# Kernel optimization log

Hardware: AMD Instinct MI355X
Metric: run time of the kernel (lower is better)

## Reference

```python
import jax, jax.numpy as jnp
import numpy as np

L, B, T, N, C, H, K, M = 2, 4, 8, 2048, 2, 64, 3, 32
DIN0, DIN1, DOUT = C + H, 2 * H, 4 * H


def setup_inputs() -> dict:
    key = jax.random.key(0)
    ks = jax.random.split(key, 24)
    s = 0.05
    p = lambda k, shape: jax.random.normal(k, shape, jnp.float32) * s
    return {
        # support matrices, roughly row-normalized random graph
        "G": jax.random.uniform(ks[0], (K, N, N), jnp.float32) * (2.0 / N),
        "x_seq": jax.random.normal(ks[1], (B, T, N, C), jnp.float32),
        "init_h": jnp.zeros((L, B, N, H), jnp.float32),
        "init_c": jnp.zeros((L, B, N, H), jnp.float32),
        "x_meta": jax.random.normal(ks[2], (B, T, M), jnp.float32),
        # layer 0 meta-learner params (dim_in = C+H)
        "lw1_0": p(ks[3], (M, 64)), "lb1_0": p(ks[4], (64,)),
        "lw2_0": p(ks[5], (64, K * DIN0 * DOUT)), "lb2_0": p(ks[6], (K * DIN0 * DOUT,)),
        "bw1_0": p(ks[7], (M, 64)), "bb1_0": p(ks[8], (64,)),
        "bw2_0": p(ks[9], (64, DOUT)), "bb2_0": p(ks[10], (DOUT,)),
        # layer 1 meta-learner params (dim_in = 2H)
        "lw1_1": p(ks[11], (M, 64)), "lb1_1": p(ks[12], (64,)),
        "lw2_1": p(ks[13], (64, K * DIN1 * DOUT)), "lb2_1": p(ks[14], (K * DIN1 * DOUT,)),
        "bw1_1": p(ks[15], (M, 64)), "bb1_1": p(ks[16], (64,)),
        "bw2_1": p(ks[17], (64, DOUT)), "bb2_1": p(ks[18], (DOUT,)),
    }


def _meta_gcn(G, x, meta, lw1, lb1, lw2, lb2, bw1, bb1, bw2, bb2):
    # x: [B, N, din] -> out: [B, N, 4H]
    Bb, Nn, din = x.shape
    # K-hop supports, concatenated along feature dim (k-major, matches torch.cat)
    sup = jnp.einsum('kij,bjd->bikd', G, x).reshape(Bb, Nn, K * din)
    W = (jax.nn.relu(meta @ lw1 + lb1) @ lw2 + lb2).reshape(Bb, K * din, DOUT)
    b = (jax.nn.relu(meta @ bw1 + bb1) @ bw2 + bb2)[:, None, :]
    return jnp.einsum('bnd,bdo->bno', sup, W) + b


def _run_layer(G, xs_t, meta_t, h0, c0, params):
    # xs_t: [T, B, N, din_x], meta_t: [T, B, M]
    def step(carry, inp):
        h, c = carry
        x_t, m_t = inp
        conv = _meta_gcn(G, jnp.concatenate([x_t, h], axis=-1), m_t, *params)
        gi, gf, go, gg = jnp.split(conv, 4, axis=-1)
        c_t = jax.nn.sigmoid(gf) * c + jax.nn.sigmoid(gi) * jnp.tanh(gg)
        h_t = jax.nn.sigmoid(go) * jnp.tanh(c_t)
        return (h_t, c_t), h_t
    (hT, cT), hs = jax.lax.scan(step, (h0, c0), (xs_t, meta_t))
    return hT, cT, hs


def reference(G, x_seq, init_h, init_c, x_meta,
              lw1_0, lb1_0, lw2_0, lb2_0, bw1_0, bb1_0, bw2_0, bb2_0,
              lw1_1, lb1_1, lw2_1, lb2_1, bw1_1, bb1_1, bw2_1, bb2_1):
    xs = jnp.transpose(x_seq, (1, 0, 2, 3))      # [T, B, N, C]
    ms = jnp.transpose(x_meta, (1, 0, 2))        # [T, B, M]
    p0 = (lw1_0, lb1_0, lw2_0, lb2_0, bw1_0, bb1_0, bw2_0, bb2_0)
    p1 = (lw1_1, lb1_1, lw2_1, lb2_1, bw1_1, bb1_1, bw2_1, bb2_1)
    h0T, c0T, hs0 = _run_layer(G, xs, ms, init_h[0], init_c[0], p0)
    h1T, c1T, _ = _run_layer(G, hs0, ms, init_h[1], init_c[1], p1)
    # [2, L, B, N, H]: [final h per layer; final c per layer]
    return jnp.stack([jnp.stack([h0T, h1T]), jnp.stack([c0T, c1T])])
```

## Files before the change

kernel.cpp:

```cpp
#include <hip/hip_runtime.h>
#include <hip/hip_bf16.h>
#include <cstdint>


typedef __hip_bfloat16 bf16;
typedef __attribute__((ext_vector_type(8))) short bf16x8;
typedef __attribute__((ext_vector_type(4))) short s16x4;
typedef __attribute__((ext_vector_type(4)))  float f32x4;
typedef __attribute__((ext_vector_type(16))) float f32x16;
typedef __attribute__((ext_vector_type(4)))  int   i32x4;
typedef __attribute__((ext_vector_type(16))) int   i32x16;

__device__ __forceinline__ short f2bf(float f) {
    unsigned u = __builtin_bit_cast(unsigned, f);
    return (short)((u + 0x7fffu + ((u >> 16) & 1u)) >> 16);
}

#define GLD_LDS(gaddr, laddr)                                                  \
    __builtin_amdgcn_global_load_lds(                                          \
        (const __attribute__((address_space(1))) void*)(gaddr),                \
        (__attribute__((address_space(3))) void*)(laddr), 16, 0, 0)

#define OFF_GSW    0u
#define OFF_GI8    25165824u
#define OFF_HFA0   37748736u
#define OFF_HFA1   38273024u
#define OFF_HFB0   38797312u
#define OFF_HFB1   39321600u
#define OFF_XS0T   39845888u
#define OFF_HS0F   40370176u
#define OFF_S0X    48758784u
#define OFF_W0SW   74711040u
#define OFF_W1SW   79429632u
#define OFF_BIAS0  85721088u
#define OFF_BIAS1  85753856u
#define OFF_C0     85786624u
#define OFF_C1     87883776u
#define WS_NEEDED  89980928u

__global__ __launch_bounds__(256) void prep_kernel(
    const float* __restrict__ G, const float* __restrict__ x_seq,
    const float* __restrict__ init_h, const float* __restrict__ init_c,
    bf16* __restrict__ Gsw, long* __restrict__ Gi8,
    long* __restrict__ hfA0, long* __restrict__ hfA1,
    bf16* __restrict__ Xs0T, float* __restrict__ c0, float* __restrict__ c1)
{
    const int T_GSB = 1572864;
    const int T_GI8 = 1572864;
    const int T_HF  = 131072;
    const int T_XS  = 262144;
    const int T_C   = 1048576;
    const int TOTAL = T_GSB + T_GI8 + T_HF + T_XS + T_C;
    int stride = gridDim.x * 256;
    for (int idx = blockIdx.x*256 + threadIdx.x; idx < TOTAL; idx += stride) {
        int i0 = idx;
        if (i0 < T_GSB) {
            int lane = i0 & 63, jc = (i0 >> 6) & 127, it32 = (i0 >> 13) & 63, k = i0 >> 19;
            int row = it32*32 + (lane & 31);
            int col = jc*16 + (lane >> 5)*8;
            const float* gp = G + ((size_t)(k*2048 + row))*2048 + col;
            f32x4 v0 = *(const f32x4*)gp, v1 = *(const f32x4*)(gp + 4);
            bf16x8 o;
            #pragma unroll
            for (int e = 0; e < 4; e++) { o[e] = f2bf(v0[e]); o[e+4] = f2bf(v1[e]); }
            *(bf16x8*)((short*)Gsw + (size_t)i0*8) = o;
            continue;
        }
        i0 -= T_GSB;
        if (i0 < T_GI8) {
            int lane = i0 & 63, jc = (i0 >> 6) & 127, it32 = (i0 >> 13) & 63, k = i0 >> 19;
            int row = it32*32 + (lane & 31);
            int col = jc*16 + (lane >> 5)*8;
            const float* gp = G + ((size_t)(k*2048 + row))*2048 + col;
            f32x4 v0 = *(const f32x4*)gp, v1 = *(const f32x4*)(gp + 4);
            long r = 0;
            #pragma unroll
            for (int e = 0; e < 4; e++) {
                int q0 = __float2int_rn(v0[e] * 130048.0f);
                int q1 = __float2int_rn(v1[e] * 130048.0f);
                q0 = q0 < 0 ? 0 : (q0 > 127 ? 127 : q0);
                q1 = q1 < 0 ? 0 : (q1 > 127 ? 127 : q1);
                r |= ((long)(unsigned char)(char)q0) << (8*e);
                r |= ((long)(unsigned char)(char)q1) << (8*(e+4));
            }
            Gi8[i0] = r;
            continue;
        }
        i0 -= T_GI8;
        if (i0 < T_HF) {
            int lane = i0 & 63, dc = (i0 >> 6) & 1, jc = (i0 >> 7) & 127;
            int b = (i0 >> 14) & 3, L = i0 >> 16;
            int j0 = jc*16 + (lane >> 5)*8, d = dc*32 + (lane & 31);
            long r = 0;
            #pragma unroll
            for (int e = 0; e < 8; e++) {
                float hv = init_h[((size_t)(L*4 + b)*2048 + j0 + e)*64 + d];
                int q = __float2int_rn(hv * 127.0f);
                q = q < -127 ? -127 : (q > 127 ? 127 : q);
                r |= ((long)(unsigned char)(char)q) << (8*e);
            }
            long* dst = (L == 0) ? hfA0 : hfA1;
            dst[i0 & 65535] = r;
            continue;
        }
        i0 -= T_HF;
        if (i0 < T_XS) {
            int n = i0 >> 11, j = i0 & 2047;
            float v = 0.f;
            if (n < 64) {
                int t = n >> 3, rm = n & 7, b = rm >> 1, cc = rm & 1;
                v = x_seq[(((size_t)b*8 + t)*2048 + j)*2 + cc];
            }
            Xs0T[i0] = __float2bfloat16(v);
            continue;
        }
        i0 -= T_XS;
        if (i0 < 524288) { c0[i0] = init_c[i0]; continue; }
        i0 -= 524288;
        c1[i0] = init_c[524288 + i0];
    }
}

__global__ __launch_bounds__(256) void metaw_kernel(
    const float* __restrict__ x_meta,
    const float* __restrict__ lw1_0, const float* __restrict__ lb1_0,
    const float* __restrict__ lw2_0, const float* __restrict__ lb2_0,
    const float* __restrict__ bw1_0, const float* __restrict__ bb1_0,
    const float* __restrict__ bw2_0, const float* __restrict__ bb2_0,
    const float* __restrict__ lw1_1, const float* __restrict__ lb1_1,
    const float* __restrict__ lw2_1, const float* __restrict__ lb2_1,
    const float* __restrict__ bw1_1, const float* __restrict__ bb1_1,
    const float* __restrict__ bw2_1, const float* __restrict__ bb2_1,
    bf16* __restrict__ W0sw, bf16* __restrict__ W1sw,
    float* __restrict__ bias0, float* __restrict__ bias1)
{
    int tid = threadIdx.x, bid = blockIdx.x;
    const float *w1, *b1v, *w2, *b2v;
    int task, r = 0;
    if (bid < 384)      { task = 0; r = bid;       w1=lw1_1; b1v=lb1_1; w2=lw2_1; b2v=lb2_1; }
    else if (bid < 582) { task = 1; r = bid - 384; w1=lw1_0; b1v=lb1_0; w2=lw2_0; b2v=lb2_0; }
    else if (bid == 582){ task = 2;                w1=bw1_0; b1v=bb1_0; w2=bw2_0; b2v=bb2_0; }
    else                { task = 3;                w1=bw1_1; b1v=bb1_1; w2=bw2_1; b2v=bb2_1; }

    __shared__ float hid[32][64];
    for (int idx = tid; idx < 2048; idx += 256) {
        int tb = idx >> 6, h = idx & 63;
        int tt = tb >> 2, b = tb & 3;
        float a = b1v[h];
        #pragma unroll
        for (int m = 0; m < 32; m++)
            a += x_meta[((size_t)b*8 + tt)*32 + m] * w1[m*64 + h];
        hid[tb][h] = fmaxf(a, 0.f);
    }
    __syncthreads();

    int o = tid;
    int RO = (task == 0) ? 98304 : (task == 1) ? 50688 : 256;
    int ro = (task >= 2) ? o : (r*256 + o);
    float col[64];
    #pragma unroll
    for (int h = 0; h < 64; h++) col[h] = w2[(size_t)h*RO + ro];
    float base = b2v[ro];

    for (int tb = 0; tb < 32; tb++) {
        float v = base;
        #pragma unroll
        for (int h = 0; h < 64; h++) v += hid[tb][h]*col[h];
        if (task == 0) {
            int rp = r, rc = rp >> 5, rr = rp & 31;
            int oc = o >> 4, l = ((rr >> 3) << 4) + (o & 15), e = rr & 7;
            W1sw[(((size_t)tb*12 + rc)*16 + oc)*512 + l*8 + e] = __float2bfloat16(v);
        } else if (task == 1) {
            int k = r/66, d = r - k*66;
            int rp = k*96 + (d < 2 ? 64 + d : d - 2);
            int rc = rp >> 5, rr = rp & 31;
            int oc = o >> 4, l = ((rr >> 3) << 4) + (o & 15), e = rr & 7;
            W0sw[(((size_t)tb*9 + rc)*16 + oc)*512 + l*8 + e] = __float2bfloat16(v);
        } else if (task == 2) bias0[tb*256 + o] = v;
        else                  bias1[tb*256 + o] = v;
    }
}

__global__ __launch_bounds__(256) void s0x_kernel(
    const short* __restrict__ Gsw, const short* __restrict__ Bm,
    bf16* __restrict__ dstB)
{
    __shared__ short lB[128 * 64];
    int bid = blockIdx.x;
    int mt = (bid & 7) * 6 + (bid >> 3);
    int kk = mt >> 4;

    int tid = threadIdx.x, lane = tid & 63, w = tid >> 6;
    int wr = w >> 1, wc = w & 1;
    int l31 = lane & 31, lhi = lane >> 5;

    int rloc = lane >> 3;
    int gsrc = ((lane & 7) ^ rloc) * 8;
    const short* Bb = Bm + gsrc;

    f32x16 acc[2][2];
    #pragma unroll
    for (int a2 = 0; a2 < 2; a2++)
        #pragma unroll
        for (int b2 = 0; b2 < 2; b2++)
            #pragma unroll
            for (int q = 0; q < 16; q++) acc[a2][b2][q] = 0.f;

    for (int kb = 0; kb < 2048; kb += 64) {
        #pragma unroll
        for (int q = 0; q < 4; q++) {
            int row = (w * 4 + q) * 8 + rloc;
            GLD_LDS(Bb + (size_t)row * 2048 + kb, &lB[(w * 4 + q) * 512]);
        }
        __syncthreads();
        #pragma unroll
        for (int ks = 0; ks < 4; ks++) {
            int jc = (kb >> 4) + ks;
            bf16x8 af[2], bf2[2];
            #pragma unroll
            for (int a2 = 0; a2 < 2; a2++) {
                int it32 = (mt & 15) * 4 + wr * 2 + a2;
                af[a2] = *(const bf16x8*)(Gsw +
                    ((((size_t)(kk * 64 + it32)) * 128 + jc) * 64 + lane) * 8);
            }
            #pragma unroll
            for (int b2 = 0; b2 < 2; b2++) {
                int r = wc * 64 + b2 * 32 + l31;
                int cb = (ks * 32 + lhi * 16) ^ ((r & 7) << 4);
                bf2[b2] = *(const bf16x8*)((const char*)lB + r * 128 + cb);
            }
            #pragma unroll
            for (int a2 = 0; a2 < 2; a2++)
                #pragma unroll
                for (int b2 = 0; b2 < 2; b2++)
                    acc[a2][b2] = __builtin_amdgcn_mfma_f32_32x32x16_bf16(
                        af[a2], bf2[b2], acc[a2][b2], 0, 0, 0);
        }
        __syncthreads();
    }

    #pragma unroll
    for (int a2 = 0; a2 < 2; a2++) {
        #pragma unroll
        for (int b2 = 0; b2 < 2; b2++) {
            int gn = wc * 64 + b2 * 32 + l31;
            if (gn >= 64) continue;
            #pragma unroll
            for (int reg = 0; reg < 16; reg++) {
                int gm = (mt & 15) * 128 + wr * 64 + a2 * 32
                         + (reg & 3) + 8 * (reg >> 2) + 4 * lhi;
                dstB[((size_t)kk * 2048 + gm) * 64 + gn] =
                    __float2bfloat16(acc[a2][b2][reg]);
            }
        }
    }
}

#define LD(P, JC)                                                              \
    do { _Pragma("unroll") for (int k = 0; k < 3; k++)                         \
            P##a[k] = Gi8[(((size_t)(k * 64 + it)) * 128 + (JC)) * 64 + lane]; \
         _Pragma("unroll") for (int dc = 0; dc < 2; dc++)                      \
            P##b[dc] = Bfr[(((size_t)(b * 128 + (JC))) * 2 + dc) * 64 + lane]; \
    } while (0)

#define CP(P)                                                                  \
    do { _Pragma("unroll") for (int k = 0; k < 3; k++)                         \
         _Pragma("unroll") for (int dc = 0; dc < 2; dc++)                      \
            acc6[k * 2 + dc] = __builtin_amdgcn_mfma_i32_32x32x16_i8(          \
                P##a[k], P##b[dc], acc6[k * 2 + dc], 0, 0, 0);                 \
    } while (0)

__device__ __forceinline__ void i8_pass(
    i32x16* acc6, const long* __restrict__ Gi8, const long* __restrict__ Bfr,
    int it, int b, int lane, int w)
{
    #pragma unroll
    for (int f = 0; f < 6; f++)
        #pragma unroll
        for (int r = 0; r < 16; r++) acc6[f][r] = 0;
    int jc0 = w * 32;
    long fAa[3], fAb[2], fBa[3], fBb[2], fCa[3], fCb[2], fDa[3], fDb[2];
    LD(fA, jc0 + 0); LD(fB, jc0 + 1); LD(fC, jc0 + 2); LD(fD, jc0 + 3);
    #pragma unroll 1
    for (int j4 = 0; j4 < 7; j4++) {
        CP(fA); LD(fA, jc0 + j4 * 4 + 4);
        CP(fB); LD(fB, jc0 + j4 * 4 + 5);
        CP(fC); LD(fC, jc0 + j4 * 4 + 6);
        CP(fD); LD(fD, jc0 + j4 * 4 + 7);
    }
    CP(fA); CP(fB); CP(fC); CP(fD);
}

__device__ __forceinline__ void reduce_sup(
    char* lds, char* SUP, i32x16* acc6, int w, int lane)
{
    int* RB = (int*)lds;
    int l31 = lane & 31, lhi = lane >> 5;
    if (w >= 2) {
        #pragma unroll
        for (int f = 0; f < 6; f++)
            #pragma unroll
            for (int qq = 0; qq < 4; qq++) {
                i32x4 v;
                #pragma unroll
                for (int r = 0; r < 4; r++) v[r] = acc6[f][qq * 4 + r];
                *(i32x4*)(RB + ((size_t)((w - 2) * 6 + f)) * 1024 + lane * 16 + qq * 4) = v;
            }
    }
    __syncthreads();
    if (w < 2) {
        #pragma unroll
        for (int f = 0; f < 6; f++)
            #pragma unroll
            for (int r = 0; r < 16; r++)
                acc6[f][r] += RB[((size_t)(w * 6 + f)) * 1024 + lane * 16 + r];
    }
    __syncthreads();
    if (w == 1) {
        #pragma unroll
        for (int f = 0; f < 6; f++)
            #pragma unroll
            for (int qq = 0; qq < 4; qq++) {
                i32x4 v;
                #pragma unroll
                for (int r = 0; r < 4; r++) v[r] = acc6[f][qq * 4 + r];
                *(i32x4*)(RB + (size_t)f * 1024 + lane * 16 + qq * 4) = v;
            }
    }
    __syncthreads();
    if (w == 0) {
        const float SCL = 1.0f / 16516096.0f;
        #pragma unroll
        for (int f = 0; f < 6; f++) {
            int k = f >> 1, dc = f & 1;
            #pragma unroll
            for (int reg = 0; reg < 16; reg++) {
                int s = acc6[f][reg] + RB[(size_t)f * 1024 + lane * 16 + reg];
                float sf = (float)s * SCL;
                int i = (reg & 3) + 8 * (reg >> 2) + 4 * lhi;
                int dpos = k * 64 + dc * 32 + l31;
                *(short*)(SUP + i * 512 + ((dpos * 2) ^ ((i & 15) << 4))) = f2bf(sf);
            }
        }
    }
    __syncthreads();
}

template<int LAYER>
__device__ __forceinline__ void step_part(
    char* lds, int idx, int t,
    const long* __restrict__ Gi8, const short* __restrict__ Sstat,
    const long* __restrict__ hs0f, const short* __restrict__ Wsw,
    const float* __restrict__ bias, float* __restrict__ cbuf,
    const long* __restrict__ hfr_in, long* __restrict__ hfr_out,
    long* __restrict__ hs0f_out, float* __restrict__ out)
{
    constexpr int NC = (LAYER == 0) ? 9 : 12;
    char* SUPs = lds + 24576;
    char* SUPr = lds + 49152;
    short* hT = (short*)(lds + 65536);
    char* hTq = lds + 69632;

    int tid = threadIdx.x, lane = tid & 63, w = tid >> 6;
    int q = idx >> 3;
    int it = (idx & 7) * 8 + (q >> 2), b = q & 3;
    int i0 = it * 32;
    int l15 = lane & 15, lg = lane >> 4;

    i32x16 acc6[6];

    if (LAYER == 0) {
        i8_pass(acc6, Gi8, hfr_in, it, b, lane, w);
        reduce_sup(lds, SUPs, acc6, w, lane);
    } else {
        i8_pass(acc6, Gi8, hfr_in, it, b, lane, w);
        reduce_sup(lds, SUPr, acc6, w, lane);
        i8_pass(acc6, Gi8, hs0f + (size_t)t * 65536, it, b, lane, w);
        reduce_sup(lds, SUPs, acc6, w, lane);
    }

    f32x4 ag[2][4];
    #pragma unroll
    for (int mi = 0; mi < 2; mi++)
        #pragma unroll
        for (int g = 0; g < 4; g++)
            #pragma unroll
            for (int r = 0; r < 4; r++) ag[mi][g][r] = 0.f;

    const short* WswT = Wsw + (size_t)(t * 4 + b) * NC * 16 * 512;

    #pragma unroll
    for (int rc = 0; rc < NC; rc++) {
        bf16x8 a0, a1;
        if (LAYER == 1) {
            int kk = rc >> 2, dq = rc & 3;
            const char* S = (dq < 2) ? SUPs : SUPr;
            int dqe = (dq < 2) ? dq : (dq - 2);
            int dpb = (kk * 64 + dqe * 32 + lg * 8) * 2;
            a0 = *(const bf16x8*)(S + l15 * 512 + (dpb ^ (l15 << 4)));
            a1 = *(const bf16x8*)(S + (l15 + 16) * 512 + (dpb ^ (l15 << 4)));
        } else {
            int kk = rc / 3, dd = rc - kk * 3;
            if (dd < 2) {
                int dpb = (kk * 64 + dd * 32 + lg * 8) * 2;
                a0 = *(const bf16x8*)(SUPs + l15 * 512 + (dpb ^ (l15 << 4)));
                a1 = *(const bf16x8*)(SUPs + (l15 + 16) * 512 + (dpb ^ (l15 << 4)));
            } else {
                #pragma unroll
                for (int e = 0; e < 8; e++) { a0[e] = 0; a1[e] = 0; }
                if (lg == 0) {
                    unsigned v0 = *(const unsigned*)(Sstat + ((size_t)kk * 2048 + i0 + l15) * 64 + t * 8 + b * 2);
                    unsigned v1 = *(const unsigned*)(Sstat + ((size_t)kk * 2048 + i0 + 16 + l15) * 64 + t * 8 + b * 2);
                    a0[0] = (short)(v0 & 0xffff); a0[1] = (short)(v0 >> 16);
                    a1[0] = (short)(v1 & 0xffff); a1[1] = (short)(v1 >> 16);
                }
            }
        }
        #pragma unroll
        for (int g = 0; g < 4; g++) {
            bf16x8 wf = *(const bf16x8*)(WswT + (((size_t)rc * 16 + (g * 4 + w)) * 64 + lane) * 8);
            ag[0][g] = __builtin_amdgcn_mfma_f32_16x16x32_bf16(a0, wf, ag[0][g], 0, 0, 0);
            ag[1][g] = __builtin_amdgcn_mfma_f32_16x16x32_bf16(a1, wf, ag[1][g], 0, 0, 0);
        }
    }

    int hcol = w * 16 + l15;
    float bia[4];
    #pragma unroll
    for (int g = 0; g < 4; g++) bia[g] = bias[(t * 4 + b) * 256 + g * 64 + hcol];

    #pragma unroll
    for (int mi = 0; mi < 2; mi++) {
        #pragma unroll
        for (int r = 0; r < 4; r++) {
            int iloc = mi * 16 + lg * 4 + r;
            int i = i0 + iloc;
            float gi = ag[mi][0][r] + bia[0];
            float gf = ag[mi][1][r] + bia[1];
            float go = ag[mi][2][r] + bia[2];
            float gg = ag[mi][3][r] + bia[3];
            size_t cidx = ((size_t)b * 2048 + i) * 64 + hcol;
            float c_old = cbuf[cidx];
            float si = 1.f / (1.f + __expf(-gi));
            float sf = 1.f / (1.f + __expf(-gf));
            float so = 1.f / (1.f + __expf(-go));
            float cn = sf * c_old + si * tanhf(gg);
            float hn = so * tanhf(cn);
            cbuf[cidx] = cn;
            hT[iloc * 64 + hcol] = f2bf(hn);
            int hq = __float2int_rn(hn * 127.0f);
            hq = hq < -127 ? -127 : (hq > 127 ? 127 : hq);
            hTq[iloc * 64 + hcol] = (char)hq;
            if (t == 7) {
                out[(((size_t)LAYER * 4 + b) * 2048 + i) * 64 + hcol]       = hn;
                out[(((size_t)(2 + LAYER) * 4 + b) * 2048 + i) * 64 + hcol] = cn;
            }
        }
    }
    __syncthreads();

    {
        int jh = tid >> 7, dc = (tid >> 6) & 1, lane6 = tid & 63;
        long r = 0;
        #pragma unroll
        for (int e = 0; e < 8; e++)
            r |= ((long)(unsigned char)hTq[(jh * 16 + (lane6 >> 5) * 8 + e) * 64
                                           + dc * 32 + (lane6 & 31)]) << (8 * e);
        size_t fidx = (((size_t)(b * 128 + it * 2 + jh)) * 2 + dc) * 64 + lane6;
        hfr_out[fidx] = r;
        if (LAYER == 0) hs0f_out[(size_t)t * 65536 + fidx] = r;
    }
}

__global__ __launch_bounds__(256) void combo_kernel(
    const long* __restrict__ Gi8, const short* __restrict__ S0x,
    const long* __restrict__ hs0f_c,
    const short* __restrict__ W0sw, const short* __restrict__ W1sw,
    const float* __restrict__ bias0, const float* __restrict__ bias1,
    float* __restrict__ c0, float* __restrict__ c1,
    long* __restrict__ hfA0, long* __restrict__ hfB0,
    long* __restrict__ hfA1, long* __restrict__ hfB1,
    long* __restrict__ hs0f, float* __restrict__ out, int tau)
{
    __shared__ char lds[71680];
    int bid = blockIdx.x;
    if (bid < 256) {
        int t = tau;
        if (t > 7) return;
        const long* hin  = (t & 1) ? hfB0 : hfA0;
        long*       hout = (t & 1) ? hfA0 : hfB0;
        step_part<0>(lds, bid, t, Gi8, S0x, nullptr, W0sw, bias0, c0,
                     hin, hout, hs0f, out);
    } else {
        int t = tau - 1;
        if (t < 0) return;
        const long* hin  = (t & 1) ? hfB1 : hfA1;
        long*       hout = (t & 1) ? hfA1 : hfB1;
        step_part<1>(lds, bid - 256, t, Gi8, nullptr, hs0f_c, W1sw, bias1, c1,
                     hin, hout, nullptr, out);
    }
}

extern "C" void kernel_launch(void* const* d_in, const int* in_sizes, int n_in,
                              void* d_out, int out_size, void* d_ws, size_t ws_size,
                              hipStream_t stream)
{
    const float* G      = (const float*)d_in[0];
    const float* x_seq  = (const float*)d_in[1];
    const float* init_h = (const float*)d_in[2];
    const float* init_c = (const float*)d_in[3];
    const float* x_meta = (const float*)d_in[4];
    const float* lw1_0 = (const float*)d_in[5],  *lb1_0 = (const float*)d_in[6];
    const float* lw2_0 = (const float*)d_in[7],  *lb2_0 = (const float*)d_in[8];
    const float* bw1_0 = (const float*)d_in[9],  *bb1_0 = (const float*)d_in[10];
    const float* bw2_0 = (const float*)d_in[11], *bb2_0 = (const float*)d_in[12];
    const float* lw1_1 = (const float*)d_in[13], *lb1_1 = (const float*)d_in[14];
    const float* lw2_1 = (const float*)d_in[15], *lb2_1 = (const float*)d_in[16];
    const float* bw1_1 = (const float*)d_in[17], *bb1_1 = (const float*)d_in[18];
    const float* bw2_1 = (const float*)d_in[19], *bb2_1 = (const float*)d_in[20];

    if (ws_size < WS_NEEDED) return;

    char* ws = (char*)d_ws;
    bf16*  Gsw   = (bf16*) (ws + OFF_GSW);
    long*  Gi8   = (long*) (ws + OFF_GI8);
    long*  hfA0  = (long*) (ws + OFF_HFA0);
    long*  hfA1  = (long*) (ws + OFF_HFA1);
    long*  hfB0  = (long*) (ws + OFF_HFB0);
    long*  hfB1  = (long*) (ws + OFF_HFB1);
    bf16*  Xs0T  = (bf16*) (ws + OFF_XS0T);
    long*  hs0f  = (long*) (ws + OFF_HS0F);
    bf16*  S0x   = (bf16*) (ws + OFF_S0X);
    bf16*  W0sw  = (bf16*) (ws + OFF_W0SW);
    bf16*  W1sw  = (bf16*) (ws + OFF_W1SW);
    float* bias0 = (float*)(ws + OFF_BIAS0);
    float* bias1 = (float*)(ws + OFF_BIAS1);
    float* c0    = (float*)(ws + OFF_C0);
    float* c1    = (float*)(ws + OFF_C1);
    float* out   = (float*)d_out;

    prep_kernel<<<4096, 256, 0, stream>>>(G, x_seq, init_h, init_c,
                                          Gsw, Gi8, hfA0, hfA1, Xs0T, c0, c1);
    metaw_kernel<<<584, 256, 0, stream>>>(x_meta,
        lw1_0, lb1_0, lw2_0, lb2_0, bw1_0, bb1_0, bw2_0, bb2_0,
        lw1_1, lb1_1, lw2_1, lb2_1, bw1_1, bb1_1, bw2_1, bb2_1,
        W0sw, W1sw, bias0, bias1);

    s0x_kernel<<<48, 256, 0, stream>>>((const short*)Gsw, (const short*)Xs0T, S0x);

    for (int tau = 0; tau < 9; tau++)
        combo_kernel<<<512, 256, 0, stream>>>(Gi8, (const short*)S0x, hs0f,
            (const short*)W0sw, (const short*)W1sw, bias0, bias1, c0, c1,
            hfA0, hfB0, hfA1, hfB1, hs0f, out, tau);
}
```

Baseline: 475.4 us.

## Fuse timestep launches into persistent kernel with grid barrier and register-resident cell state

Replaces the nine per-timestep combo_kernel launches with one persistent kernel of 512 blocks that loops over timesteps and synchronizes through a global atomic counter barrier. The LSTM cell state now lives in registers across steps instead of being read and written in global memory, and the prep copy of init_c is removed. Hidden states are kept per timestep in larger buffers instead of ping-ponging. The aim is to remove launch gaps and c-state traffic. The grid barrier relies on all 512 blocks being co-resident (launch_bounds 256,2 on 256 CUs), which risks deadlock or spin overhead if occupancy falls short.

```diff
diff --git a/kernel.cpp b/kernel.cpp
--- a/kernel.cpp
+++ b/kernel.cpp
@@ -23,34 +23,31 @@
 
 #define OFF_GSW    0u
 #define OFF_GI8    25165824u
-#define OFF_HFA0   37748736u
-#define OFF_HFA1   38273024u
-#define OFF_HFB0   38797312u
-#define OFF_HFB1   39321600u
-#define OFF_XS0T   39845888u
-#define OFF_HS0F   40370176u
-#define OFF_S0X    48758784u
-#define OFF_W0SW   74711040u
-#define OFF_W1SW   79429632u
-#define OFF_BIAS0  85721088u
-#define OFF_BIAS1  85753856u
-#define OFF_C0     85786624u
-#define OFF_C1     87883776u
-#define WS_NEEDED  89980928u
+#define OFF_HR0    37748736u
+#define OFF_HR1    42467328u
+#define OFF_HS0F   47185920u
+#define OFF_XS0T   51380224u
+#define OFF_S0X    51904512u
+#define OFF_W0SW   52690944u
+#define OFF_W1SW   57409536u
+#define OFF_BIAS0  63700992u
+#define OFF_BIAS1  63733760u
+#define OFF_BAR    63766528u
+#define WS_NEEDED  63767552u
 
 __global__ __launch_bounds__(256) void prep_kernel(
     const float* __restrict__ G, const float* __restrict__ x_seq,
-    const float* __restrict__ init_h, const float* __restrict__ init_c,
+    const float* __restrict__ init_h,
     bf16* __restrict__ Gsw, long* __restrict__ Gi8,
-    long* __restrict__ hfA0, long* __restrict__ hfA1,
-    bf16* __restrict__ Xs0T, float* __restrict__ c0, float* __restrict__ c1)
-{
+    long* __restrict__ hr0, long* __restrict__ hr1,
+    bf16* __restrict__ Xs0T, unsigned* __restrict__ bar)
+{
+    if (blockIdx.x == 0 && threadIdx.x == 0) *bar = 0u;
     const int T_GSB = 1572864;
     const int T_GI8 = 1572864;
     const int T_HF  = 131072;
     const int T_XS  = 262144;
-    const int T_C   = 1048576;
-    const int TOTAL = T_GSB + T_GI8 + T_HF + T_XS + T_C;
+    const int TOTAL = T_GSB + T_GI8 + T_HF + T_XS;
     int stride = gridDim.x * 256;
     for (int idx = blockIdx.x*256 + threadIdx.x; idx < TOTAL; idx += stride) {
         int i0 = idx;
@@ -99,12 +96,12 @@
                 q = q < -127 ? -127 : (q > 127 ? 127 : q);
                 r |= ((long)(unsigned char)(char)q) << (8*e);
             }
-            long* dst = (L == 0) ? hfA0 : hfA1;
+            long* dst = (L == 0) ? hr0 : hr1;
             dst[i0 & 65535] = r;
             continue;
         }
         i0 -= T_HF;
-        if (i0 < T_XS) {
+        {
             int n = i0 >> 11, j = i0 & 2047;
             float v = 0.f;
             if (n < 64) {
@@ -112,12 +109,7 @@
                 v = x_seq[(((size_t)b*8 + t)*2048 + j)*2 + cc];
             }
             Xs0T[i0] = __float2bfloat16(v);
-            continue;
-        }
-        i0 -= T_XS;
-        if (i0 < 524288) { c0[i0] = init_c[i0]; continue; }
-        i0 -= 524288;
-        c1[i0] = init_c[524288 + i0];
+        }
     }
 }
 
@@ -347,11 +339,11 @@
 }
 
 template<int LAYER>
-__device__ __forceinline__ void step_part(
-    char* lds, int idx, int t,
+__device__ __forceinline__ void step_body(
+    char* lds, int it, int b, int t,
     const long* __restrict__ Gi8, const short* __restrict__ Sstat,
-    const long* __restrict__ hs0f, const short* __restrict__ Wsw,
-    const float* __restrict__ bias, float* __restrict__ cbuf,
+    const long* __restrict__ hs0f_t, const short* __restrict__ Wsw,
+    const float* __restrict__ bias, float (&creg)[8],
     const long* __restrict__ hfr_in, long* __restrict__ hfr_out,
     long* __restrict__ hs0f_out, float* __restrict__ out)
 {
@@ -362,8 +354,6 @@
     char* hTq = lds + 69632;
 
     int tid = threadIdx.x, lane = tid & 63, w = tid >> 6;
-    int q = idx >> 3;
-    int it = (idx & 7) * 8 + (q >> 2), b = q & 3;
     int i0 = it * 32;
     int l15 = lane & 15, lg = lane >> 4;
 
@@ -375,7 +365,7 @@
     } else {
         i8_pass(acc6, Gi8, hfr_in, it, b, lane, w);
         reduce_sup(lds, SUPr, acc6, w, lane);
-        i8_pass(acc6, Gi8, hs0f + (size_t)t * 65536, it, b, lane, w);
+        i8_pass(acc6, Gi8, hs0f_t, it, b, lane, w);
         reduce_sup(lds, SUPs, acc6, w, lane);
     }
 
@@ -439,14 +429,13 @@
             float gf = ag[mi][1][r] + bia[1];
             float go = ag[mi][2][r] + bia[2];
             float gg = ag[mi][3][r] + bia[3];
-            size_t cidx = ((size_t)b * 2048 + i) * 64 + hcol;
-            float c_old = cbuf[cidx];
+            float c_old = creg[mi * 4 + r];
             float si = 1.f / (1.f + __expf(-gi));
             float sf = 1.f / (1.f + __expf(-gf));
             float so = 1.f / (1.f + __expf(-go));
             float cn = sf * c_old + si * tanhf(gg);
             float hn = so * tanhf(cn);
-            cbuf[cidx] = cn;
+            creg[mi * 4 + r] = cn;
             hT[iloc * 64 + hcol] = f2bf(hn);
             int hq = __float2int_rn(hn * 127.0f);
             hq = hq < -127 ? -127 : (hq > 127 ? 127 : hq);
@@ -468,36 +457,69 @@
                                            + dc * 32 + (lane6 & 31)]) << (8 * e);
         size_t fidx = (((size_t)(b * 128 + it * 2 + jh)) * 2 + dc) * 64 + lane6;
         hfr_out[fidx] = r;
-        if (LAYER == 0) hs0f_out[(size_t)t * 65536 + fidx] = r;
-    }
-}
-
-__global__ __launch_bounds__(256) void combo_kernel(
+        if (LAYER == 0) hs0f_out[fidx] = r;
+    }
+}
+
+__global__ __launch_bounds__(256, 2) void persist_combo(
     const long* __restrict__ Gi8, const short* __restrict__ S0x,
-    const long* __restrict__ hs0f_c,
     const short* __restrict__ W0sw, const short* __restrict__ W1sw,
     const float* __restrict__ bias0, const float* __restrict__ bias1,
-    float* __restrict__ c0, float* __restrict__ c1,
-    long* __restrict__ hfA0, long* __restrict__ hfB0,
-    long* __restrict__ hfA1, long* __restrict__ hfB1,
-    long* __restrict__ hs0f, float* __restrict__ out, int tau)
+    const float* __restrict__ init_c,
+    long* __restrict__ hr0, long* __restrict__ hr1,
+    long* __restrict__ hs0f, float* __restrict__ out,
+    unsigned* __restrict__ bar)
 {
     __shared__ char lds[71680];
     int bid = blockIdx.x;
-    if (bid < 256) {
-        int t = tau;
-        if (t > 7) return;
-        const long* hin  = (t & 1) ? hfB0 : hfA0;
-        long*       hout = (t & 1) ? hfA0 : hfB0;
-        step_part<0>(lds, bid, t, Gi8, S0x, nullptr, W0sw, bias0, c0,
-                     hin, hout, hs0f, out);
-    } else {
-        int t = tau - 1;
-        if (t < 0) return;
-        const long* hin  = (t & 1) ? hfB1 : hfA1;
-        long*       hout = (t & 1) ? hfA1 : hfB1;
-        step_part<1>(lds, bid - 256, t, Gi8, nullptr, hs0f_c, W1sw, bias1, c1,
-                     hin, hout, nullptr, out);
+    int layer = bid >> 8;
+    int idx = bid & 255;
+    int q = idx >> 3;
+    int it = (idx & 7) * 8 + (q >> 2), b = q & 3;
+    int i0 = it * 32;
+
+    int tid = threadIdx.x, lane = tid & 63, w = tid >> 6;
+    int l15 = lane & 15, lg = lane >> 4;
+    int hcol = w * 16 + l15;
+
+    float creg[8];
+    #pragma unroll
+    for (int mi = 0; mi < 2; mi++)
+        #pragma unroll
+        for (int r = 0; r < 4; r++) {
+            int i = i0 + mi * 16 + lg * 4 + r;
+            creg[mi * 4 + r] = init_c[(((size_t)layer * 4 + b) * 2048 + i) * 64 + hcol];
+        }
+
+    #pragma unroll 1
+    for (int tau = 0; tau < 9; tau++) {
+        int t = (layer == 0) ? tau : tau - 1;
+        if (t >= 0 && t <= 7) {
+            if (layer == 0) {
+                step_body<0>(lds, it, b, t, Gi8, S0x, nullptr, W0sw, bias0,
+                             creg, hr0 + (size_t)t * 65536,
+                             hr0 + (size_t)(t + 1) * 65536,
+                             hs0f + (size_t)t * 65536, out);
+            } else {
+                step_body<1>(lds, it, b, t, Gi8, nullptr,
+                             hs0f + (size_t)t * 65536, W1sw, bias1,
+                             creg, hr1 + (size_t)t * 65536,
+                             hr1 + (size_t)(t + 1) * 65536, nullptr, out);
+            }
+        }
+        if (tau < 8) {
+            asm volatile("s_waitcnt vmcnt(0)" ::: "memory");
+            __syncthreads();
+            if (tid == 0) {
+                __hip_atomic_fetch_add(bar, 1u, __ATOMIC_RELEASE,
+                                       __HIP_MEMORY_SCOPE_AGENT);
+                unsigned tgt = 512u * (unsigned)(tau + 1);
+                while (__hip_atomic_load(bar, __ATOMIC_RELAXED,
+                                         __HIP_MEMORY_SCOPE_AGENT) < tgt)
+                    __builtin_amdgcn_s_sleep(4);
+            }
+            __syncthreads();
+        }
     }
 }
 
@@ -524,23 +546,20 @@
     char* ws = (char*)d_ws;
     bf16*  Gsw   = (bf16*) (ws + OFF_GSW);
     long*  Gi8   = (long*) (ws + OFF_GI8);
-    long*  hfA0  = (long*) (ws + OFF_HFA0);
-    long*  hfA1  = (long*) (ws + OFF_HFA1);
-    long*  hfB0  = (long*) (ws + OFF_HFB0);
-    long*  hfB1  = (long*) (ws + OFF_HFB1);
+    long*  hr0   = (long*) (ws + OFF_HR0);
+    long*  hr1   = (long*) (ws + OFF_HR1);
+    long*  hs0f  = (long*) (ws + OFF_HS0F);
     bf16*  Xs0T  = (bf16*) (ws + OFF_XS0T);
-    long*  hs0f  = (long*) (ws + OFF_HS0F);
     bf16*  S0x   = (bf16*) (ws + OFF_S0X);
     bf16*  W0sw  = (bf16*) (ws + OFF_W0SW);
     bf16*  W1sw  = (bf16*) (ws + OFF_W1SW);
     float* bias0 = (float*)(ws + OFF_BIAS0);
     float* bias1 = (float*)(ws + OFF_BIAS1);
-    float* c0    = (float*)(ws + OFF_C0);
-    float* c1    = (float*)(ws + OFF_C1);
+    unsigned* bar= (unsigned*)(ws + OFF_BAR);
     float* out   = (float*)d_out;
 
-    prep_kernel<<<4096, 256, 0, stream>>>(G, x_seq, init_h, init_c,
-                                          Gsw, Gi8, hfA0, hfA1, Xs0T, c0, c1);
+    prep_kernel<<<4096, 256, 0, stream>>>(G, x_seq, init_h,
+                                          Gsw, Gi8, hr0, hr1, Xs0T, bar);
     metaw_kernel<<<584, 256, 0, stream>>>(x_meta,
         lw1_0, lb1_0, lw2_0, lb2_0, bw1_0, bb1_0, bw2_0, bb2_0,
         lw1_1, lb1_1, lw2_1, lb2_1, bw1_1, bb1_1, bw2_1, bb2_1,
@@ -548,8 +567,7 @@
 
     s0x_kernel<<<48, 256, 0, stream>>>((const short*)Gsw, (const short*)Xs0T, S0x);
 
-    for (int tau = 0; tau < 9; tau++)
-        combo_kernel<<<512, 256, 0, stream>>>(Gi8, (const short*)S0x, hs0f,
-            (const short*)W0sw, (const short*)W1sw, bias0, bias1, c0, c1,
-            hfA0, hfB0, hfA1, hfB1, hs0f, out, tau);
-}
+    persist_combo<<<512, 256, 0, stream>>>(Gi8, (const short*)S0x,
+        (const short*)W0sw, (const short*)W1sw, bias0, bias1, init_c,
+        hr0, hr1, hs0f, out, bar);
+}
```

Result: slower. 970.8 us (+104.2%).
